# Kernel optimization log

Measured on AMD Instinct MI355X. Metric: run time of the kernel, lower is better.

Reference implementation:

```python
import jax, jax.numpy as jnp
import numpy as np

N_NODES = 100000
N_EDGES = 600000
D_IN = 128
D_OUT = 128


def setup_inputs() -> dict:
    key = jax.random.key(0)
    k1, k2, k3 = jax.random.split(key, 3)
    x = jax.random.normal(k1, (N_NODES, D_IN), dtype=jnp.float32)
    edge_index = jax.random.randint(k2, (2, N_EDGES), 0, N_NODES, dtype=jnp.int64)
    # Glorot-style init for the GCN weight, zero bias (PyG defaults)
    W = jax.random.normal(k3, (D_IN, D_OUT), dtype=jnp.float32) * (1.0 / np.sqrt(D_IN))
    b = jnp.zeros((D_OUT,), dtype=jnp.float32)
    return {"x": x, "edge_index": edge_index, "W": W, "b": b}


def reference(x, edge_index, W, b):
    """GCNConv: out = D^{-1/2} (A + I) D^{-1/2} (x @ W) + b."""
    n = x.shape[0]
    self_loop = jnp.arange(n, dtype=edge_index.dtype)
    src = jnp.concatenate([edge_index[0], self_loop])  # [E + N]
    dst = jnp.concatenate([edge_index[1], self_loop])

    xw = x @ W  # [N, D_OUT] dense transform before aggregation

    # symmetric normalization with self-loops
    deg = jax.ops.segment_sum(jnp.ones_like(dst, dtype=x.dtype), dst, num_segments=n)
    dinv = jnp.where(deg > 0, jax.lax.rsqrt(deg), 0.0)
    norm = dinv[src] * dinv[dst]  # [E + N]

    # gather source features, scale, scatter-add to destinations
    msgs = norm[:, None] * xw[src]  # [E + N, D_OUT]
    out = jax.ops.segment_sum(msgs, dst, num_segments=n)
    return out + b
```

## Files before the change

### kernel.cpp

```cpp
#include <hip/hip_runtime.h>
#include <hip/hip_bf16.h>
#include <stdint.h>

#define N_NODES 100000
#define N_EDGES 600000
#define D 128
#define WT_LD 136
#define SCAN_NBLK ((N_NODES + 255) / 256)
#define CAP 32

typedef unsigned short u16;
typedef uint32_t u32;
typedef __attribute__((ext_vector_type(8))) short bf16x8;
typedef __attribute__((ext_vector_type(4))) float f32x4;

union bfpack { bf16x8 v; u16 s[8]; };

__device__ __forceinline__ float bf2f(u16 u) {
    union { u32 i; float f; } v; v.i = ((u32)u) << 16; return v.f;
}
__device__ __forceinline__ u16 f2bf(float f) {
    union { float f; u32 i; } v; v.f = f;
    u32 lsb = (v.i >> 16) & 1u;
    return (u16)((v.i + 0x7fffu + lsb) >> 16);
}

__global__ __launch_bounds__(256) void k_init(const u32* __restrict__ xu,
                                              const int* __restrict__ ei,
                                              int* __restrict__ deg,
                                              int* __restrict__ flags) {
    int t = threadIdx.x;
    int idx = blockIdx.x * 256 + t;
    if (idx < N_NODES) deg[idx] = 0;
    if (blockIdx.x == 0) {
        __shared__ int cnt[2];
        if (t < 2) cnt[t] = 0;
        __syncthreads();
        const u32* eu = (const u32*)ei;
        int bad = 0, zc = 0;
        for (int i = 0; i < 16; i++) {
            u32 w = xu[t + 256 * i];
            int e0 = (w >> 7) & 0xFF, e1 = (w >> 23) & 0xFF;
            bad += ((e0 == 0 || e0 == 0xFF) ? 1 : 0) + ((e1 == 0 || e1 == 0xFF) ? 1 : 0);
            zc += (eu[2 * (t + 256 * i) + 1] == 0) ? 1 : 0;
        }
        atomicAdd(&cnt[0], bad);
        atomicAdd(&cnt[1], zc);
        __syncthreads();
        if (t == 0) { flags[0] = cnt[0] > 8 ? 1 : 0; flags[1] = cnt[1] > 2048 ? 1 : 0; }
    }
}

__global__ __launch_bounds__(256) void k_build(const int* __restrict__ ei,
                                               const int* __restrict__ flags,
                                               int* __restrict__ cnt,
                                               int* __restrict__ csr) {
    int t = blockIdx.x * 256 + threadIdx.x;
    if (2 * t >= N_EDGES) return;
    int s0, s1, d0, d1;
    if (flags[1]) {
        int4 sv = *(const int4*)(ei + 4 * t);
        int4 dv = *(const int4*)(ei + 2 * N_EDGES + 4 * t);
        s0 = sv.x; s1 = sv.z; d0 = dv.x; d1 = dv.z;
    } else {
        int2 sv = *(const int2*)(ei + 2 * t);
        int2 dv = *(const int2*)(ei + N_EDGES + 2 * t);
        s0 = sv.x; s1 = sv.y; d0 = dv.x; d1 = dv.y;
    }
    if ((unsigned)s0 >= N_NODES) s0 = 0;
    if ((unsigned)s1 >= N_NODES) s1 = 0;
    if ((unsigned)d0 >= N_NODES) d0 = 0;
    if ((unsigned)d1 >= N_NODES) d1 = 0;
    int slot0 = atomicAdd(&cnt[d0], 1);
    if (slot0 < CAP) csr[(long)d0 * CAP + slot0] = s0;
    int slot1 = atomicAdd(&cnt[d1], 1);
    if (slot1 < CAP) csr[(long)d1 * CAP + slot1] = s1;
}

__global__ void k_hist(const int* __restrict__ ei, const int* __restrict__ flags,
                       int* __restrict__ deg) {
    int e = blockIdx.x * 256 + threadIdx.x;
    if (e < N_EDGES) {
        int d = flags[1] ? ei[2 * (N_EDGES + e)] : ei[N_EDGES + e];
        if ((unsigned)d >= N_NODES) d = 0;
        atomicAdd(&deg[d], 1);
    }
}

__global__ __launch_bounds__(256) void k_reduce(const int* __restrict__ deg,
                                                int* __restrict__ bsum) {
    __shared__ int ws[4];
    int t = threadIdx.x, lane = t & 63, wave = t >> 6;
    int idx = blockIdx.x * 256 + t;
    int v = (idx < N_NODES) ? deg[idx] : 0;
    for (int o = 32; o > 0; o >>= 1) v += __shfl_down(v, o, 64);
    if (lane == 0) ws[wave] = v;
    __syncthreads();
    if (t == 0) bsum[blockIdx.x] = ws[0] + ws[1] + ws[2] + ws[3];
}

__global__ __launch_bounds__(512) void k_scanbs(const int* __restrict__ bsum,
                                                int* __restrict__ bpre,
                                                int* __restrict__ offs) {
    __shared__ int lds[512];
    int t = threadIdx.x;
    int v = (t < SCAN_NBLK) ? bsum[t] : 0;
    lds[t] = v;
    __syncthreads();
    for (int off = 1; off < 512; off <<= 1) {
        int u = (t >= off) ? lds[t - off] : 0;
        __syncthreads();
        lds[t] += u;
        __syncthreads();
    }
    if (t < SCAN_NBLK) bpre[t] = (t == 0) ? 0 : lds[t - 1];
    if (t == SCAN_NBLK - 1) offs[N_NODES] = lds[t];
}

__global__ __launch_bounds__(256) void k_apply(const int* __restrict__ deg,
                                               const int* __restrict__ bpre,
                                               int* __restrict__ offs,
                                               int* __restrict__ cursor) {
    __shared__ int ws[4];
    int t = threadIdx.x, lane = t & 63, wave = t >> 6;
    int idx = blockIdx.x * 256 + t;
    int d = (idx < N_NODES) ? deg[idx] : 0;
    int v = d;
    for (int o = 1; o < 64; o <<= 1) {
        int u = __shfl_up(v, o, 64);
        if (lane >= o) v += u;
    }
    if (lane == 63) ws[wave] = v;
    __syncthreads();
    int add = 0;
    for (int w = 0; w < wave; w++) add += ws[w];
    int excl = bpre[blockIdx.x] + add + v - d;
    if (idx < N_NODES) {
        offs[idx] = excl;
        cursor[idx] = excl;
    }
}

__global__ void k_scatter(const int* __restrict__ ei, const int* __restrict__ flags,
                          int* __restrict__ cursor, int* __restrict__ csr) {
    int e = blockIdx.x * 256 + threadIdx.x;
    if (e < N_EDGES) {
        int s, d;
        if (flags[1]) { s = ei[2 * e]; d = ei[2 * (N_EDGES + e)]; }
        else          { s = ei[e];     d = ei[N_EDGES + e]; }
        if ((unsigned)s >= N_NODES) s = 0;
        if ((unsigned)d >= N_NODES) d = 0;
        int slot = atomicAdd(&cursor[d], 1);
        csr[slot] = s;
    }
}

__global__ __launch_bounds__(256) void k_gemm(const int* __restrict__ flags,
                                              const void* __restrict__ xp,
                                              const void* __restrict__ Wp,
                                              const int* __restrict__ deg,
                                              u16* __restrict__ xw) {
    __shared__ u16 Wt[2][128 * WT_LD];
    int t = threadIdx.x, wave = t >> 6, lane = t & 63;
    int m16 = lane & 15, q = lane >> 4;
    int row0 = blockIdx.x * 128 + wave * 32;
    int f32 = flags[0];
    f32x4 acc[2][8];
    for (int a = 0; a < 2; a++)
        for (int c = 0; c < 8; c++) acc[a][c] = (f32x4){0.f, 0.f, 0.f, 0.f};

    int r0 = row0 + m16;      if (r0 > N_NODES - 1) r0 = N_NODES - 1;
    int r1 = row0 + 16 + m16; if (r1 > N_NODES - 1) r1 = N_NODES - 1;

    if (f32) {
        const float* Wf = (const float*)Wp;
        const float* xf = (const float*)xp;
        for (int i = 0; i < 64; i++) {
            int idx = t + i * 256, k = idx >> 7, n = idx & 127;
            float w = Wf[idx];
            u16 h = f2bf(w);
            Wt[0][n * WT_LD + k] = h;
            Wt[1][n * WT_LD + k] = f2bf(w - bf2f(h));
        }
        __syncthreads();
        for (int kt = 0; kt < 4; kt++) {
            int kbase = kt * 32 + q * 8;
            float4 u0 = *(const float4*)(xf + (long)r0 * D + kbase);
            float4 u1 = *(const float4*)(xf + (long)r0 * D + kbase + 4);
            float4 v0 = *(const float4*)(xf + (long)r1 * D + kbase);
            float4 v1 = *(const float4*)(xf + (long)r1 * D + kbase + 4);
            float t0[8] = {u0.x, u0.y, u0.z, u0.w, u1.x, u1.y, u1.z, u1.w};
            float t1[8] = {v0.x, v0.y, v0.z, v0.w, v1.x, v1.y, v1.z, v1.w};
            bfpack h0, l0, h1, l1;
            for (int j = 0; j < 8; j++) {
                u16 a = f2bf(t0[j]); h0.s[j] = a; l0.s[j] = f2bf(t0[j] - bf2f(a));
                u16 b = f2bf(t1[j]); h1.s[j] = b; l1.s[j] = f2bf(t1[j] - bf2f(b));
            }
            for (int ct = 0; ct < 8; ct++) {
                bf16x8 bh = *(const bf16x8*)(&Wt[0][(ct * 16 + m16) * WT_LD + kbase]);
                bf16x8 bl = *(const bf16x8*)(&Wt[1][(ct * 16 + m16) * WT_LD + kbase]);
                acc[0][ct] = __builtin_amdgcn_mfma_f32_16x16x32_bf16(h0.v, bh, acc[0][ct], 0, 0, 0);
                acc[0][ct] = __builtin_amdgcn_mfma_f32_16x16x32_bf16(l0.v, bh, acc[0][ct], 0, 0, 0);
                acc[0][ct] = __builtin_amdgcn_mfma_f32_16x16x32_bf16(h0.v, bl, acc[0][ct], 0, 0, 0);
                acc[1][ct] = __builtin_amdgcn_mfma_f32_16x16x32_bf16(h1.v, bh, acc[1][ct], 0, 0, 0);
                acc[1][ct] = __builtin_amdgcn_mfma_f32_16x16x32_bf16(l1.v, bh, acc[1][ct], 0, 0, 0);
                acc[1][ct] = __builtin_amdgcn_mfma_f32_16x16x32_bf16(h1.v, bl, acc[1][ct], 0, 0, 0);
            }
        }
    } else {
        const u16* W16 = (const u16*)Wp;
        const u16* x16 = (const u16*)xp;
        for (int i = 0; i < 64; i++) {
            int idx = t + i * 256, k = idx >> 7, n = idx & 127;
            Wt[0][n * WT_LD + k] = W16[idx];
        }
        __syncthreads();
        for (int kt = 0; kt < 4; kt++) {
            int kbase = kt * 32 + q * 8;
            bf16x8 a0 = *(const bf16x8*)(x16 + (long)r0 * D + kbase);
            bf16x8 a1 = *(const bf16x8*)(x16 + (long)r1 * D + kbase);
            for (int ct = 0; ct < 8; ct++) {
                bf16x8 b = *(const bf16x8*)(&Wt[0][(ct * 16 + m16) * WT_LD + kbase]);
                acc[0][ct] = __builtin_amdgcn_mfma_f32_16x16x32_bf16(a0, b, acc[0][ct], 0, 0, 0);
                acc[1][ct] = __builtin_amdgcn_mfma_f32_16x16x32_bf16(a1, b, acc[1][ct], 0, 0, 0);
            }
        }
    }
    for (int a = 0; a < 2; a++)
        for (int r = 0; r < 4; r++) {
            int row = row0 + a * 16 + q * 4 + r;
            if (row < N_NODES) {
                float dr = rsqrtf((float)(deg[row] + 1));
                for (int ct = 0; ct < 8; ct++)
                    xw[(long)row * D + ct * 16 + m16] = f2bf(dr * acc[a][ct][r]);
            }
        }
}

__global__ __launch_bounds__(256) void k_agg_bkt(const int* __restrict__ flags,
                                                 const u16* __restrict__ xw,
                                                 const int* __restrict__ csr,
                                                 const int* __restrict__ cnt,
                                                 const void* __restrict__ bp,
                                                 void* __restrict__ outp) {
    int wave = threadIdx.x >> 6, lane = threadIdx.x & 63;
    int n = blockIdx.x * 4 + wave;
    int c = lane * 2;
    int deg = cnt[n];
    float dn = rsqrtf((float)(deg + 1));
    int m = deg < CAP ? deg : CAP;
    const int* base = csr + (long)n * CAP;
    u32 pv = *(const u32*)(xw + (long)n * D + c);
    float ax = bf2f((u16)pv), ay = bf2f((u16)(pv >> 16));
    for (int j = 0; j < m; j += 4) {
        int4 qi = *(const int4*)(base + j);
        bool v1 = (j + 1) < m, v2 = (j + 2) < m, v3 = (j + 3) < m;
        int s0 = qi.x;
        int s1 = v1 ? qi.y : n;
        int s2 = v2 ? qi.z : n;
        int s3 = v3 ? qi.w : n;
        u32 g0 = *(const u32*)(xw + (long)s0 * D + c);
        u32 g1 = *(const u32*)(xw + (long)s1 * D + c);
        u32 g2 = *(const u32*)(xw + (long)s2 * D + c);
        u32 g3 = *(const u32*)(xw + (long)s3 * D + c);
        ax += bf2f((u16)g0);          ay += bf2f((u16)(g0 >> 16));
        ax += v1 ? bf2f((u16)g1) : 0.f; ay += v1 ? bf2f((u16)(g1 >> 16)) : 0.f;
        ax += v2 ? bf2f((u16)g2) : 0.f; ay += v2 ? bf2f((u16)(g2 >> 16)) : 0.f;
        ax += v3 ? bf2f((u16)g3) : 0.f; ay += v3 ? bf2f((u16)(g3 >> 16)) : 0.f;
    }
    if (flags[0]) {
        const float* bf_ = (const float*)bp;
        float2 bb = *(const float2*)(bf_ + c);
        float* outf = (float*)outp;
        *(float2*)(outf + (long)n * D + c) = make_float2(dn * ax + bb.x, dn * ay + bb.y);
    } else {
        const u16* b16 = (const u16*)bp;
        u32 bb = *(const u32*)(b16 + c);
        u16* out16 = (u16*)outp;
        u32 o = (u32)f2bf(dn * ax + bf2f((u16)bb)) |
                ((u32)f2bf(dn * ay + bf2f((u16)(bb >> 16))) << 16);
        *(u32*)(out16 + (long)n * D + c) = o;
    }
}

__global__ __launch_bounds__(256) void k_agg_csr(const int* __restrict__ flags,
                                                 const u16* __restrict__ xw,
                                                 const int* __restrict__ csr,
                                                 const int* __restrict__ offs,
                                                 const void* __restrict__ bp,
                                                 void* __restrict__ outp) {
    int wave = threadIdx.x >> 6, lane = threadIdx.x & 63;
    int n = blockIdx.x * 4 + wave;
    int c = lane * 2;
    int e0 = offs[n], e1 = offs[n + 1];
    float dn = rsqrtf((float)(e1 - e0 + 1));
    u32 pv = *(const u32*)(xw + (long)n * D + c);
    float ax = bf2f((u16)pv), ay = bf2f((u16)(pv >> 16));
    int j = e0;
    for (; j + 4 <= e1; j += 4) {
        int s0 = csr[j], s1 = csr[j + 1], s2 = csr[j + 2], s3 = csr[j + 3];
        u32 q0 = *(const u32*)(xw + (long)s0 * D + c);
        u32 q1 = *(const u32*)(xw + (long)s1 * D + c);
        u32 q2 = *(const u32*)(xw + (long)s2 * D + c);
        u32 q3 = *(const u32*)(xw + (long)s3 * D + c);
        ax += bf2f((u16)q0) + bf2f((u16)q1) + bf2f((u16)q2) + bf2f((u16)q3);
        ay += bf2f((u16)(q0 >> 16)) + bf2f((u16)(q1 >> 16)) +
              bf2f((u16)(q2 >> 16)) + bf2f((u16)(q3 >> 16));
    }
    for (; j < e1; j++) {
        int s = csr[j];
        u32 qv = *(const u32*)(xw + (long)s * D + c);
        ax += bf2f((u16)qv);
        ay += bf2f((u16)(qv >> 16));
    }
    if (flags[0]) {
        const float* bf_ = (const float*)bp;
        float2 bb = *(const float2*)(bf_ + c);
        float* outf = (float*)outp;
        *(float2*)(outf + (long)n * D + c) = make_float2(dn * ax + bb.x, dn * ay + bb.y);
    } else {
        const u16* b16 = (const u16*)bp;
        u32 bb = *(const u32*)(b16 + c);
        u16* out16 = (u16*)outp;
        u32 o = (u32)f2bf(dn * ax + bf2f((u16)bb)) |
                ((u32)f2bf(dn * ay + bf2f((u16)(bb >> 16))) << 16);
        *(u32*)(out16 + (long)n * D + c) = o;
    }
}

extern "C" void kernel_launch(void* const* d_in, const int* in_sizes, int n_in,
                              void* d_out, int out_size, void* d_ws, size_t ws_size,
                              hipStream_t stream) {
    const void* x  = d_in[0];
    const int* ei  = (const int*)d_in[1];
    const void* W  = d_in[2];
    const void* b  = d_in[3];
    char* ws = (char*)d_ws;

    const size_t BUCKET_NEED = 64 + 400000 + (size_t)N_NODES * CAP * 4 + (size_t)N_NODES * D * 2 + 64;
    if (ws_size >= BUCKET_NEED) {
        int* flags = (int*)(ws + 0);
        int* cnt   = (int*)(ws + 64);
        int* csr   = (int*)(ws + 400128);
        u16* xw    = (u16*)(ws + 400128 + (size_t)N_NODES * CAP * 4);
        k_init<<<SCAN_NBLK, 256, 0, stream>>>((const u32*)x, ei, cnt, flags);
        k_build<<<(N_EDGES / 2 + 255) / 256, 256, 0, stream>>>(ei, flags, cnt, csr);
        k_gemm<<<(N_NODES + 127) / 128, 256, 0, stream>>>(flags, x, W, cnt, xw);
        k_agg_bkt<<<N_NODES / 4, 256, 0, stream>>>(flags, xw, csr, cnt, b, d_out);
    } else {
        int*   flags  = (int*)(ws + 0);
        int*   deg    = (int*)(ws + 64);
        int*   offs   = (int*)(ws + 400064);
        int*   cursor = (int*)(ws + 800068);
        int*   csr    = (int*)(ws + 1200068);
        int*   bsum   = (int*)(ws + 3600068);
        int*   bpre   = (int*)(ws + 3601636);
        u16*   xw     = (u16*)(ws + 3603216);
        k_init<<<SCAN_NBLK, 256, 0, stream>>>((const u32*)x, ei, deg, flags);
        k_hist<<<(N_EDGES + 255) / 256, 256, 0, stream>>>(ei, flags, deg);
        k_reduce<<<SCAN_NBLK, 256, 0, stream>>>(deg, bsum);
        k_scanbs<<<1, 512, 0, stream>>>(bsum, bpre, offs);
        k_apply<<<SCAN_NBLK, 256, 0, stream>>>(deg, bpre, offs, cursor);
        k_gemm<<<(N_NODES + 127) / 128, 256, 0, stream>>>(flags, x, W, deg, xw);
        k_scatter<<<(N_EDGES + 255) / 256, 256, 0, stream>>>(ei, flags, cursor, csr);
        k_agg_csr<<<N_NODES / 4, 256, 0, stream>>>(flags, xw, csr, offs, b, d_out);
    }
}
```

Before: 204.8 us.

## Drop W low-part MFMA, widen gather unroll, add nontemporal loads/stores, remove CSR fallback

The fp32 GEMM path now rounds W to a single bf16 copy and skips the h*lo(W) MFMA term, cutting MFMA count and LDS footprint by a third. The bucketed aggregation unrolls to 8 gathered neighbors per iteration for more memory-level parallelism. Edge-index and x loads and output stores become nontemporal, and the workspace-size fallback CSR path is deleted. The trade-off is lower precision in x@W and no fallback when the workspace is too small.

```diff
diff --git a/kernel.cpp b/kernel.cpp
--- a/kernel.cpp
+++ b/kernel.cpp
@@ -6,13 +6,16 @@
 #define N_EDGES 600000
 #define D 128
 #define WT_LD 136
-#define SCAN_NBLK ((N_NODES + 255) / 256)
+#define NBLK ((N_NODES + 255) / 256)
 #define CAP 32
 
 typedef unsigned short u16;
 typedef uint32_t u32;
+typedef unsigned long long u64;
 typedef __attribute__((ext_vector_type(8))) short bf16x8;
 typedef __attribute__((ext_vector_type(4))) float f32x4;
+typedef __attribute__((ext_vector_type(4))) int int4v;
+typedef __attribute__((ext_vector_type(2))) int int2v;
 
 union bfpack { bf16x8 v; u16 s[8]; };
 
@@ -27,14 +30,14 @@
 
 __global__ __launch_bounds__(256) void k_init(const u32* __restrict__ xu,
                                               const int* __restrict__ ei,
-                                              int* __restrict__ deg,
+                                              int* __restrict__ cnt,
                                               int* __restrict__ flags) {
     int t = threadIdx.x;
     int idx = blockIdx.x * 256 + t;
-    if (idx < N_NODES) deg[idx] = 0;
+    if (idx < N_NODES) cnt[idx] = 0;
     if (blockIdx.x == 0) {
-        __shared__ int cnt[2];
-        if (t < 2) cnt[t] = 0;
+        __shared__ int c[2];
+        if (t < 2) c[t] = 0;
         __syncthreads();
         const u32* eu = (const u32*)ei;
         int bad = 0, zc = 0;
@@ -44,10 +47,10 @@
             bad += ((e0 == 0 || e0 == 0xFF) ? 1 : 0) + ((e1 == 0 || e1 == 0xFF) ? 1 : 0);
             zc += (eu[2 * (t + 256 * i) + 1] == 0) ? 1 : 0;
         }
-        atomicAdd(&cnt[0], bad);
-        atomicAdd(&cnt[1], zc);
-        __syncthreads();
-        if (t == 0) { flags[0] = cnt[0] > 8 ? 1 : 0; flags[1] = cnt[1] > 2048 ? 1 : 0; }
+        atomicAdd(&c[0], bad);
+        atomicAdd(&c[1], zc);
+        __syncthreads();
+        if (t == 0) { flags[0] = c[0] > 8 ? 1 : 0; flags[1] = c[1] > 2048 ? 1 : 0; }
     }
 }
 
@@ -59,12 +62,12 @@
     if (2 * t >= N_EDGES) return;
     int s0, s1, d0, d1;
     if (flags[1]) {
-        int4 sv = *(const int4*)(ei + 4 * t);
-        int4 dv = *(const int4*)(ei + 2 * N_EDGES + 4 * t);
+        int4v sv = __builtin_nontemporal_load((const int4v*)(ei + 4 * t));
+        int4v dv = __builtin_nontemporal_load((const int4v*)(ei + 2 * N_EDGES + 4 * t));
         s0 = sv.x; s1 = sv.z; d0 = dv.x; d1 = dv.z;
     } else {
-        int2 sv = *(const int2*)(ei + 2 * t);
-        int2 dv = *(const int2*)(ei + N_EDGES + 2 * t);
+        int2v sv = __builtin_nontemporal_load((const int2v*)(ei + 2 * t));
+        int2v dv = __builtin_nontemporal_load((const int2v*)(ei + N_EDGES + 2 * t));
         s0 = sv.x; s1 = sv.y; d0 = dv.x; d1 = dv.y;
     }
     if ((unsigned)s0 >= N_NODES) s0 = 0;
@@ -77,90 +80,12 @@
     if (slot1 < CAP) csr[(long)d1 * CAP + slot1] = s1;
 }
 
-__global__ void k_hist(const int* __restrict__ ei, const int* __restrict__ flags,
-                       int* __restrict__ deg) {
-    int e = blockIdx.x * 256 + threadIdx.x;
-    if (e < N_EDGES) {
-        int d = flags[1] ? ei[2 * (N_EDGES + e)] : ei[N_EDGES + e];
-        if ((unsigned)d >= N_NODES) d = 0;
-        atomicAdd(&deg[d], 1);
-    }
-}
-
-__global__ __launch_bounds__(256) void k_reduce(const int* __restrict__ deg,
-                                                int* __restrict__ bsum) {
-    __shared__ int ws[4];
-    int t = threadIdx.x, lane = t & 63, wave = t >> 6;
-    int idx = blockIdx.x * 256 + t;
-    int v = (idx < N_NODES) ? deg[idx] : 0;
-    for (int o = 32; o > 0; o >>= 1) v += __shfl_down(v, o, 64);
-    if (lane == 0) ws[wave] = v;
-    __syncthreads();
-    if (t == 0) bsum[blockIdx.x] = ws[0] + ws[1] + ws[2] + ws[3];
-}
-
-__global__ __launch_bounds__(512) void k_scanbs(const int* __restrict__ bsum,
-                                                int* __restrict__ bpre,
-                                                int* __restrict__ offs) {
-    __shared__ int lds[512];
-    int t = threadIdx.x;
-    int v = (t < SCAN_NBLK) ? bsum[t] : 0;
-    lds[t] = v;
-    __syncthreads();
-    for (int off = 1; off < 512; off <<= 1) {
-        int u = (t >= off) ? lds[t - off] : 0;
-        __syncthreads();
-        lds[t] += u;
-        __syncthreads();
-    }
-    if (t < SCAN_NBLK) bpre[t] = (t == 0) ? 0 : lds[t - 1];
-    if (t == SCAN_NBLK - 1) offs[N_NODES] = lds[t];
-}
-
-__global__ __launch_bounds__(256) void k_apply(const int* __restrict__ deg,
-                                               const int* __restrict__ bpre,
-                                               int* __restrict__ offs,
-                                               int* __restrict__ cursor) {
-    __shared__ int ws[4];
-    int t = threadIdx.x, lane = t & 63, wave = t >> 6;
-    int idx = blockIdx.x * 256 + t;
-    int d = (idx < N_NODES) ? deg[idx] : 0;
-    int v = d;
-    for (int o = 1; o < 64; o <<= 1) {
-        int u = __shfl_up(v, o, 64);
-        if (lane >= o) v += u;
-    }
-    if (lane == 63) ws[wave] = v;
-    __syncthreads();
-    int add = 0;
-    for (int w = 0; w < wave; w++) add += ws[w];
-    int excl = bpre[blockIdx.x] + add + v - d;
-    if (idx < N_NODES) {
-        offs[idx] = excl;
-        cursor[idx] = excl;
-    }
-}
-
-__global__ void k_scatter(const int* __restrict__ ei, const int* __restrict__ flags,
-                          int* __restrict__ cursor, int* __restrict__ csr) {
-    int e = blockIdx.x * 256 + threadIdx.x;
-    if (e < N_EDGES) {
-        int s, d;
-        if (flags[1]) { s = ei[2 * e]; d = ei[2 * (N_EDGES + e)]; }
-        else          { s = ei[e];     d = ei[N_EDGES + e]; }
-        if ((unsigned)s >= N_NODES) s = 0;
-        if ((unsigned)d >= N_NODES) d = 0;
-        int slot = atomicAdd(&cursor[d], 1);
-        csr[slot] = s;
-    }
-}
-
 __global__ __launch_bounds__(256) void k_gemm(const int* __restrict__ flags,
                                               const void* __restrict__ xp,
                                               const void* __restrict__ Wp,
                                               const int* __restrict__ deg,
                                               u16* __restrict__ xw) {
-    __shared__ u16 Wt[2][128 * WT_LD];
+    __shared__ u16 Wt[128 * WT_LD];
     int t = threadIdx.x, wave = t >> 6, lane = t & 63;
     int m16 = lane & 15, q = lane >> 4;
     int row0 = blockIdx.x * 128 + wave * 32;
@@ -177,18 +102,15 @@
         const float* xf = (const float*)xp;
         for (int i = 0; i < 64; i++) {
             int idx = t + i * 256, k = idx >> 7, n = idx & 127;
-            float w = Wf[idx];
-            u16 h = f2bf(w);
-            Wt[0][n * WT_LD + k] = h;
-            Wt[1][n * WT_LD + k] = f2bf(w - bf2f(h));
+            Wt[n * WT_LD + k] = f2bf(Wf[idx]);
         }
         __syncthreads();
         for (int kt = 0; kt < 4; kt++) {
             int kbase = kt * 32 + q * 8;
-            float4 u0 = *(const float4*)(xf + (long)r0 * D + kbase);
-            float4 u1 = *(const float4*)(xf + (long)r0 * D + kbase + 4);
-            float4 v0 = *(const float4*)(xf + (long)r1 * D + kbase);
-            float4 v1 = *(const float4*)(xf + (long)r1 * D + kbase + 4);
+            f32x4 u0 = __builtin_nontemporal_load((const f32x4*)(xf + (long)r0 * D + kbase));
+            f32x4 u1 = __builtin_nontemporal_load((const f32x4*)(xf + (long)r0 * D + kbase + 4));
+            f32x4 v0 = __builtin_nontemporal_load((const f32x4*)(xf + (long)r1 * D + kbase));
+            f32x4 v1 = __builtin_nontemporal_load((const f32x4*)(xf + (long)r1 * D + kbase + 4));
             float t0[8] = {u0.x, u0.y, u0.z, u0.w, u1.x, u1.y, u1.z, u1.w};
             float t1[8] = {v0.x, v0.y, v0.z, v0.w, v1.x, v1.y, v1.z, v1.w};
             bfpack h0, l0, h1, l1;
@@ -197,14 +119,11 @@
                 u16 b = f2bf(t1[j]); h1.s[j] = b; l1.s[j] = f2bf(t1[j] - bf2f(b));
             }
             for (int ct = 0; ct < 8; ct++) {
-                bf16x8 bh = *(const bf16x8*)(&Wt[0][(ct * 16 + m16) * WT_LD + kbase]);
-                bf16x8 bl = *(const bf16x8*)(&Wt[1][(ct * 16 + m16) * WT_LD + kbase]);
+                bf16x8 bh = *(const bf16x8*)(&Wt[(ct * 16 + m16) * WT_LD + kbase]);
                 acc[0][ct] = __builtin_amdgcn_mfma_f32_16x16x32_bf16(h0.v, bh, acc[0][ct], 0, 0, 0);
                 acc[0][ct] = __builtin_amdgcn_mfma_f32_16x16x32_bf16(l0.v, bh, acc[0][ct], 0, 0, 0);
-                acc[0][ct] = __builtin_amdgcn_mfma_f32_16x16x32_bf16(h0.v, bl, acc[0][ct], 0, 0, 0);
                 acc[1][ct] = __builtin_amdgcn_mfma_f32_16x16x32_bf16(h1.v, bh, acc[1][ct], 0, 0, 0);
                 acc[1][ct] = __builtin_amdgcn_mfma_f32_16x16x32_bf16(l1.v, bh, acc[1][ct], 0, 0, 0);
-                acc[1][ct] = __builtin_amdgcn_mfma_f32_16x16x32_bf16(h1.v, bl, acc[1][ct], 0, 0, 0);
             }
         }
     } else {
@@ -212,7 +131,7 @@
         const u16* x16 = (const u16*)xp;
         for (int i = 0; i < 64; i++) {
             int idx = t + i * 256, k = idx >> 7, n = idx & 127;
-            Wt[0][n * WT_LD + k] = W16[idx];
+            Wt[n * WT_LD + k] = W16[idx];
         }
         __syncthreads();
         for (int kt = 0; kt < 4; kt++) {
@@ -220,7 +139,7 @@
             bf16x8 a0 = *(const bf16x8*)(x16 + (long)r0 * D + kbase);
             bf16x8 a1 = *(const bf16x8*)(x16 + (long)r1 * D + kbase);
             for (int ct = 0; ct < 8; ct++) {
-                bf16x8 b = *(const bf16x8*)(&Wt[0][(ct * 16 + m16) * WT_LD + kbase]);
+                bf16x8 b = *(const bf16x8*)(&Wt[(ct * 16 + m16) * WT_LD + kbase]);
                 acc[0][ct] = __builtin_amdgcn_mfma_f32_16x16x32_bf16(a0, b, acc[0][ct], 0, 0, 0);
                 acc[1][ct] = __builtin_amdgcn_mfma_f32_16x16x32_bf16(a1, b, acc[1][ct], 0, 0, 0);
             }
@@ -237,12 +156,12 @@
         }
 }
 
-__global__ __launch_bounds__(256) void k_agg_bkt(const int* __restrict__ flags,
-                                                 const u16* __restrict__ xw,
-                                                 const int* __restrict__ csr,
-                                                 const int* __restrict__ cnt,
-                                                 const void* __restrict__ bp,
-                                                 void* __restrict__ outp) {
+__global__ __launch_bounds__(256) void k_agg(const int* __restrict__ flags,
+                                             const u16* __restrict__ xw,
+                                             const int* __restrict__ csr,
+                                             const int* __restrict__ cnt,
+                                             const void* __restrict__ bp,
+                                             void* __restrict__ outp) {
     int wave = threadIdx.x >> 6, lane = threadIdx.x & 63;
     int n = blockIdx.x * 4 + wave;
     int c = lane * 2;
@@ -252,79 +171,50 @@
     const int* base = csr + (long)n * CAP;
     u32 pv = *(const u32*)(xw + (long)n * D + c);
     float ax = bf2f((u16)pv), ay = bf2f((u16)(pv >> 16));
-    for (int j = 0; j < m; j += 4) {
-        int4 qi = *(const int4*)(base + j);
+    for (int j = 0; j < m; j += 8) {
+        int4v qa = *(const int4v*)(base + j);
+        int4v qb = *(const int4v*)(base + j + 4);
         bool v1 = (j + 1) < m, v2 = (j + 2) < m, v3 = (j + 3) < m;
-        int s0 = qi.x;
-        int s1 = v1 ? qi.y : n;
-        int s2 = v2 ? qi.z : n;
-        int s3 = v3 ? qi.w : n;
+        bool v4 = (j + 4) < m, v5 = (j + 5) < m, v6 = (j + 6) < m, v7 = (j + 7) < m;
+        int s0 = qa.x;
+        int s1 = v1 ? qa.y : n;
+        int s2 = v2 ? qa.z : n;
+        int s3 = v3 ? qa.w : n;
+        int s4 = v4 ? qb.x : n;
+        int s5 = v5 ? qb.y : n;
+        int s6 = v6 ? qb.z : n;
+        int s7 = v7 ? qb.w : n;
         u32 g0 = *(const u32*)(xw + (long)s0 * D + c);
         u32 g1 = *(const u32*)(xw + (long)s1 * D + c);
         u32 g2 = *(const u32*)(xw + (long)s2 * D + c);
         u32 g3 = *(const u32*)(xw + (long)s3 * D + c);
-        ax += bf2f((u16)g0);          ay += bf2f((u16)(g0 >> 16));
+        u32 g4 = *(const u32*)(xw + (long)s4 * D + c);
+        u32 g5 = *(const u32*)(xw + (long)s5 * D + c);
+        u32 g6 = *(const u32*)(xw + (long)s6 * D + c);
+        u32 g7 = *(const u32*)(xw + (long)s7 * D + c);
+        ax += bf2f((u16)g0);            ay += bf2f((u16)(g0 >> 16));
         ax += v1 ? bf2f((u16)g1) : 0.f; ay += v1 ? bf2f((u16)(g1 >> 16)) : 0.f;
         ax += v2 ? bf2f((u16)g2) : 0.f; ay += v2 ? bf2f((u16)(g2 >> 16)) : 0.f;
         ax += v3 ? bf2f((u16)g3) : 0.f; ay += v3 ? bf2f((u16)(g3 >> 16)) : 0.f;
+        ax += v4 ? bf2f((u16)g4) : 0.f; ay += v4 ? bf2f((u16)(g4 >> 16)) : 0.f;
+        ax += v5 ? bf2f((u16)g5) : 0.f; ay += v5 ? bf2f((u16)(g5 >> 16)) : 0.f;
+        ax += v6 ? bf2f((u16)g6) : 0.f; ay += v6 ? bf2f((u16)(g6 >> 16)) : 0.f;
+        ax += v7 ? bf2f((u16)g7) : 0.f; ay += v7 ? bf2f((u16)(g7 >> 16)) : 0.f;
     }
     if (flags[0]) {
         const float* bf_ = (const float*)bp;
         float2 bb = *(const float2*)(bf_ + c);
         float* outf = (float*)outp;
-        *(float2*)(outf + (long)n * D + c) = make_float2(dn * ax + bb.x, dn * ay + bb.y);
+        union { float2 f; u64 u; } o;
+        o.f = make_float2(dn * ax + bb.x, dn * ay + bb.y);
+        __builtin_nontemporal_store(o.u, (u64*)(outf + (long)n * D + c));
     } else {
         const u16* b16 = (const u16*)bp;
         u32 bb = *(const u32*)(b16 + c);
         u16* out16 = (u16*)outp;
         u32 o = (u32)f2bf(dn * ax + bf2f((u16)bb)) |
                 ((u32)f2bf(dn * ay + bf2f((u16)(bb >> 16))) << 16);
-        *(u32*)(out16 + (long)n * D + c) = o;
-    }
-}
-
-__global__ __launch_bounds__(256) void k_agg_csr(const int* __restrict__ flags,
-                                                 const u16* __restrict__ xw,
-                                                 const int* __restrict__ csr,
-                                                 const int* __restrict__ offs,
-                                                 const void* __restrict__ bp,
-                                                 void* __restrict__ outp) {
-    int wave = threadIdx.x >> 6, lane = threadIdx.x & 63;
-    int n = blockIdx.x * 4 + wave;
-    int c = lane * 2;
-    int e0 = offs[n], e1 = offs[n + 1];
-    float dn = rsqrtf((float)(e1 - e0 + 1));
-    u32 pv = *(const u32*)(xw + (long)n * D + c);
-    float ax = bf2f((u16)pv), ay = bf2f((u16)(pv >> 16));
-    int j = e0;
-    for (; j + 4 <= e1; j += 4) {
-        int s0 = csr[j], s1 = csr[j + 1], s2 = csr[j + 2], s3 = csr[j + 3];
-        u32 q0 = *(const u32*)(xw + (long)s0 * D + c);
-        u32 q1 = *(const u32*)(xw + (long)s1 * D + c);
-        u32 q2 = *(const u32*)(xw + (long)s2 * D + c);
-        u32 q3 = *(const u32*)(xw + (long)s3 * D + c);
-        ax += bf2f((u16)q0) + bf2f((u16)q1) + bf2f((u16)q2) + bf2f((u16)q3);
-        ay += bf2f((u16)(q0 >> 16)) + bf2f((u16)(q1 >> 16)) +
-              bf2f((u16)(q2 >> 16)) + bf2f((u16)(q3 >> 16));
-    }
-    for (; j < e1; j++) {
-        int s = csr[j];
-        u32 qv = *(const u32*)(xw + (long)s * D + c);
-        ax += bf2f((u16)qv);
-        ay += bf2f((u16)(qv >> 16));
-    }
-    if (flags[0]) {
-        const float* bf_ = (const float*)bp;
-        float2 bb = *(const float2*)(bf_ + c);
-        float* outf = (float*)outp;
-        *(float2*)(outf + (long)n * D + c) = make_float2(dn * ax + bb.x, dn * ay + bb.y);
-    } else {
-        const u16* b16 = (const u16*)bp;
-        u32 bb = *(const u32*)(b16 + c);
-        u16* out16 = (u16*)outp;
-        u32 o = (u32)f2bf(dn * ax + bf2f((u16)bb)) |
-                ((u32)f2bf(dn * ay + bf2f((u16)(bb >> 16))) << 16);
-        *(u32*)(out16 + (long)n * D + c) = o;
+        __builtin_nontemporal_store(o, (u32*)(out16 + (long)n * D + c));
     }
 }
 
@@ -337,32 +227,13 @@
     const void* b  = d_in[3];
     char* ws = (char*)d_ws;
 
-    const size_t BUCKET_NEED = 64 + 400000 + (size_t)N_NODES * CAP * 4 + (size_t)N_NODES * D * 2 + 64;
-    if (ws_size >= BUCKET_NEED) {
-        int* flags = (int*)(ws + 0);
-        int* cnt   = (int*)(ws + 64);
-        int* csr   = (int*)(ws + 400128);
-        u16* xw    = (u16*)(ws + 400128 + (size_t)N_NODES * CAP * 4);
-        k_init<<<SCAN_NBLK, 256, 0, stream>>>((const u32*)x, ei, cnt, flags);
-        k_build<<<(N_EDGES / 2 + 255) / 256, 256, 0, stream>>>(ei, flags, cnt, csr);
-        k_gemm<<<(N_NODES + 127) / 128, 256, 0, stream>>>(flags, x, W, cnt, xw);
-        k_agg_bkt<<<N_NODES / 4, 256, 0, stream>>>(flags, xw, csr, cnt, b, d_out);
-    } else {
-        int*   flags  = (int*)(ws + 0);
-        int*   deg    = (int*)(ws + 64);
-        int*   offs   = (int*)(ws + 400064);
-        int*   cursor = (int*)(ws + 800068);
-        int*   csr    = (int*)(ws + 1200068);
-        int*   bsum   = (int*)(ws + 3600068);
-        int*   bpre   = (int*)(ws + 3601636);
-        u16*   xw     = (u16*)(ws + 3603216);
-        k_init<<<SCAN_NBLK, 256, 0, stream>>>((const u32*)x, ei, deg, flags);
-        k_hist<<<(N_EDGES + 255) / 256, 256, 0, stream>>>(ei, flags, deg);
-        k_reduce<<<SCAN_NBLK, 256, 0, stream>>>(deg, bsum);
-        k_scanbs<<<1, 512, 0, stream>>>(bsum, bpre, offs);
-        k_apply<<<SCAN_NBLK, 256, 0, stream>>>(deg, bpre, offs, cursor);
-        k_gemm<<<(N_NODES + 127) / 128, 256, 0, stream>>>(flags, x, W, deg, xw);
-        k_scatter<<<(N_EDGES + 255) / 256, 256, 0, stream>>>(ei, flags, cursor, csr);
-        k_agg_csr<<<N_NODES / 4, 256, 0, stream>>>(flags, xw, csr, offs, b, d_out);
-    }
-}
+    int* flags = (int*)(ws + 0);
+    int* cnt   = (int*)(ws + 64);
+    int* csr   = (int*)(ws + 400128);
+    u16* xw    = (u16*)(ws + 400128 + (size_t)N_NODES * CAP * 4);
+
+    k_init<<<NBLK, 256, 0, stream>>>((const u32*)x, ei, cnt, flags);
+    k_build<<<(N_EDGES / 2 + 255) / 256, 256, 0, stream>>>(ei, flags, cnt, csr);
+    k_gemm<<<(N_NODES + 127) / 128, 256, 0, stream>>>(flags, x, W, cnt, xw);
+    k_agg<<<N_NODES / 4, 256, 0, stream>>>(flags, xw, csr, cnt, b, d_out);
+}
```

Result: no change. 205.4 us (+0.3%).
